# Performance work log

Measured on AMD Instinct MI355X. Metric: run time of the kernel, lower is better.

The kernel has to match this reference:

```python
import jax, jax.numpy as jnp
import numpy as np

N_NODES = 50000
N_EDGES = 800000
D = 128
N_LAYERS = 4
NUM_GRAPHS = 128
BN_EPS = 1e-5


def setup_inputs() -> dict:
    key = jax.random.key(0)
    ks = jax.random.split(key, 10)
    x = jax.random.normal(ks[0], (N_NODES, D), dtype=jnp.float32)
    edge_index = jax.random.randint(ks[1], (2, N_EDGES), 0, N_NODES, dtype=jnp.int64)
    batch = jnp.sort(jax.random.randint(ks[2], (N_NODES,), 0, NUM_GRAPHS, dtype=jnp.int64))
    # GINConv MLP params: Linear(D->D), ReLU, Linear(D->D); stacked over layers.
    scale = 1.0 / np.sqrt(D)
    W1 = jax.random.normal(ks[3], (N_LAYERS, D, D), dtype=jnp.float32) * scale
    b1 = jnp.zeros((N_LAYERS, D), dtype=jnp.float32)
    W2 = jax.random.normal(ks[4], (N_LAYERS, D, D), dtype=jnp.float32) * scale
    b2 = jnp.zeros((N_LAYERS, D), dtype=jnp.float32)
    eps = jnp.zeros((N_LAYERS,), dtype=jnp.float32)  # train_eps=True, init 0
    bn_gamma = jnp.ones((N_LAYERS - 1, D), dtype=jnp.float32)
    bn_beta = jnp.zeros((N_LAYERS - 1, D), dtype=jnp.float32)
    return {"x": x, "edge_index": edge_index, "batch": batch,
            "W1": W1, "b1": b1, "W2": W2, "b2": b2, "eps": eps,
            "bn_gamma": bn_gamma, "bn_beta": bn_beta}


def reference(x, edge_index, batch, W1, b1, W2, b2, eps, bn_gamma, bn_beta):
    src, dst = edge_index[0], edge_index[1]
    h = x
    for i in range(N_LAYERS):
        # GINConv: MLP((1+eps)*x_i + sum_{j->i} x_j)
        agg = jax.ops.segment_sum(h[src], dst, num_segments=N_NODES)  # [N, D]
        z = (1.0 + eps[i]) * h + agg
        z = jnp.maximum(z @ W1[i] + b1[i], 0.0) @ W2[i] + b2[i]
        if i < N_LAYERS - 1:
            # BatchNorm1d (training-mode batch statistics) + ReLU
            mu = jnp.mean(z, axis=0)
            var = jnp.var(z, axis=0)
            z = (z - mu) * jax.lax.rsqrt(var + BN_EPS) * bn_gamma[i] + bn_beta[i]
            z = jnp.maximum(z, 0.0)
        h = z
    # global_add_pool
    return jax.ops.segment_sum(h, batch, num_segments=NUM_GRAPHS)  # [G, D]
```

## Files before the change

### kernel.cpp

```cpp
#include <hip/hip_runtime.h>

#define N_NODES 50000
#define N_EDGES 800000
#define D 128
#define NUM_GRAPHS 128

typedef __attribute__((ext_vector_type(8)))  short bfrag8;
typedef __attribute__((ext_vector_type(16))) float f32x16;

__device__ __forceinline__ float4 f4zero() { return make_float4(0.f, 0.f, 0.f, 0.f); }

__device__ __forceinline__ unsigned short f2bf(float f) {
    unsigned u = __float_as_uint(f);
    unsigned r = (u + 0x7fffu + ((u >> 16) & 1u)) >> 16;
    return (unsigned short)r;
}
__device__ __forceinline__ float bf2f(unsigned short b) {
    return __uint_as_float(((unsigned)b) << 16);
}
__device__ __forceinline__ void acc8(float* a, uint4 r) {
    a[0] += __uint_as_float(r.x << 16);
    a[1] += __uint_as_float(r.x & 0xffff0000u);
    a[2] += __uint_as_float(r.y << 16);
    a[3] += __uint_as_float(r.y & 0xffff0000u);
    a[4] += __uint_as_float(r.z << 16);
    a[5] += __uint_as_float(r.z & 0xffff0000u);
    a[6] += __uint_as_float(r.w << 16);
    a[7] += __uint_as_float(r.w & 0xffff0000u);
}

__global__ __launch_bounds__(256) void prep_kernel(
    const float* __restrict__ W1, const float* __restrict__ W2,
    const float* __restrict__ x, short* __restrict__ Wt,
    ushort4* __restrict__ Hb, int* __restrict__ deg, float* __restrict__ stats,
    float* __restrict__ outZero)
{
    int b = blockIdx.x, t = threadIdx.x;
    if (b < 512) {
        int idx = b * 256 + t;
        int m = idx >> 14, rem = idx & 16383;
        int k = rem >> 7, n = rem & 127;
        const float* W = (m < 4) ? (W1 + (size_t)m * 16384)
                                 : (W2 + (size_t)(m - 4) * 16384);
        Wt[(size_t)m * 16384 + n * 128 + k] = (short)f2bf(W[k * 128 + n]);
    } else if (b < 6762) {
        int i = (b - 512) * 256 + t;
        float4 v = ((const float4*)x)[i];
        Hb[i] = make_ushort4(f2bf(v.x), f2bf(v.y), f2bf(v.z), f2bf(v.w));
    } else if (b < 6958) {
        int i = (b - 6762) * 256 + t;
        if (i < N_NODES) deg[i] = 0;
    } else if (b < 6982) {
        int i = (b - 6958) * 256 + t;
        stats[i] = 0.f;
    } else if (b < 7046) {
        int i = (b - 6982) * 256 + t;
        outZero[i] = 0.f;
    } else {
        if (t < 64) ((unsigned*)Hb)[(size_t)N_NODES * 64 + t] = 0u;
    }
}

__global__ __launch_bounds__(256) void hist_kernel(
    const int* __restrict__ dst, int* __restrict__ deg,
    unsigned short* __restrict__ edge_pos)
{
    int e = blockIdx.x * 256 + threadIdx.x;
    if (e < N_EDGES) edge_pos[e] = (unsigned short)atomicAdd(&deg[dst[e]], 1);
}

__global__ __launch_bounds__(256) void scan_block_kernel(
    const int* __restrict__ deg, int* __restrict__ row_ptr,
    int* __restrict__ blockSum)
{
    __shared__ int wsum[4];
    int t = threadIdx.x, b = blockIdx.x;
    int i = b * 256 + t;
    int v = (i < N_NODES) ? ((deg[i] + 7) & ~7) : 0;
    int lane = t & 63, wid = t >> 6;
    #pragma unroll
    for (int off = 1; off < 64; off <<= 1) {
        int u = __shfl_up(v, off, 64);
        if (lane >= off) v += u;
    }
    if (lane == 63) wsum[wid] = v;
    __syncthreads();
    int add = 0;
    for (int w = 0; w < wid; ++w) add += wsum[w];
    v += add;
    if (i < N_NODES) row_ptr[i + 1] = v;
    if (t == 255) blockSum[b] = v;
}

__global__ __launch_bounds__(256) void scan_fixup_kernel(
    const int* __restrict__ blockSum, int* __restrict__ row_ptr, int nb)
{
    __shared__ int wsum[4];
    __shared__ int sbuf[256];
    int t = threadIdx.x, b = blockIdx.x;
    int v = (t < nb) ? blockSum[t] : 0;
    int lane = t & 63, wid = t >> 6;
    #pragma unroll
    for (int off = 1; off < 64; off <<= 1) {
        int u = __shfl_up(v, off, 64);
        if (lane >= off) v += u;
    }
    if (lane == 63) wsum[wid] = v;
    __syncthreads();
    int add = 0;
    for (int w = 0; w < wid; ++w) add += wsum[w];
    sbuf[t] = v + add;
    __syncthreads();
    if (b == 0 && t == 0) row_ptr[0] = 0;
    if (b > 0) {
        int off = sbuf[b - 1];
        int i = b * 256 + t;
        if (i < N_NODES) row_ptr[i + 1] += off;
    }
}

__global__ __launch_bounds__(256) void fill_kernel(
    const int* __restrict__ src, const int* __restrict__ dst,
    const int* __restrict__ row_ptr, const unsigned short* __restrict__ edge_pos,
    const int* __restrict__ deg, unsigned short* __restrict__ csr_src)
{
    int b = blockIdx.x, t = threadIdx.x;
    if (b < 3125) {
        int e = b * 256 + t;
        if (e < N_EDGES)
            csr_src[row_ptr[dst[e]] + (int)edge_pos[e]] = (unsigned short)src[e];
    } else {
        int n = (b - 3125) * 256 + t;
        if (n < N_NODES) {
            int e0 = row_ptr[n] + deg[n];
            int e1 = row_ptr[n + 1];
            for (int j = e0; j < e1; ++j)
                csr_src[j] = (unsigned short)N_NODES;
        }
    }
}

__global__ __launch_bounds__(256) void bnapply_kernel(
    uint4* __restrict__ H, const float* __restrict__ stats,
    const float* __restrict__ gamma, const float* __restrict__ beta)
{
    __shared__ float sa[128], sb[128];
    int tid = threadIdx.x;
    if (tid < 128) {
        float s = 0.f, q = 0.f;
        #pragma unroll
        for (int k = 0; k < 8; ++k) {
            s += stats[k * 256 + tid];
            q += stats[k * 256 + 128 + tid];
        }
        const float invN = 1.0f / (float)N_NODES;
        float m = s * invN;
        float a = gamma[tid] * rsqrtf(q * invN - m * m + 1e-5f);
        sa[tid] = a;
        sb[tid] = beta[tid] - m * a;
    }
    __syncthreads();
    int id = blockIdx.x * 256 + tid;
    int c0 = (id & 15) * 8;
    uint4 u = H[id];
    float lo, hi;
    lo = fmaxf(sa[c0 + 0] * __uint_as_float(u.x << 16)          + sb[c0 + 0], 0.f);
    hi = fmaxf(sa[c0 + 1] * __uint_as_float(u.x & 0xffff0000u) + sb[c0 + 1], 0.f);
    u.x = (unsigned)f2bf(lo) | ((unsigned)f2bf(hi) << 16);
    lo = fmaxf(sa[c0 + 2] * __uint_as_float(u.y << 16)          + sb[c0 + 2], 0.f);
    hi = fmaxf(sa[c0 + 3] * __uint_as_float(u.y & 0xffff0000u) + sb[c0 + 3], 0.f);
    u.y = (unsigned)f2bf(lo) | ((unsigned)f2bf(hi) << 16);
    lo = fmaxf(sa[c0 + 4] * __uint_as_float(u.z << 16)          + sb[c0 + 4], 0.f);
    hi = fmaxf(sa[c0 + 5] * __uint_as_float(u.z & 0xffff0000u) + sb[c0 + 5], 0.f);
    u.z = (unsigned)f2bf(lo) | ((unsigned)f2bf(hi) << 16);
    lo = fmaxf(sa[c0 + 6] * __uint_as_float(u.w << 16)          + sb[c0 + 6], 0.f);
    hi = fmaxf(sa[c0 + 7] * __uint_as_float(u.w & 0xffff0000u) + sb[c0 + 7], 0.f);
    u.w = (unsigned)f2bf(lo) | ((unsigned)f2bf(hi) << 16);
    H[id] = u;
}

__global__ __launch_bounds__(256, 4) void gather_kernel(
    const uint4* __restrict__ H, const int* __restrict__ row_ptr,
    const unsigned short* __restrict__ csr, const float* __restrict__ epsp,
    uint4* __restrict__ A)
{
    int node = blockIdx.x * 16 + (threadIdx.x >> 4);
    int lane = threadIdx.x & 15;
    float eps1 = 1.0f + *epsp;
    int beg = row_ptr[node], end = row_ptr[node + 1];

    uint4 hv = H[(size_t)node * 16 + lane];
    float acc[8];
    acc[0] = eps1 * __uint_as_float(hv.x << 16);
    acc[1] = eps1 * __uint_as_float(hv.x & 0xffff0000u);
    acc[2] = eps1 * __uint_as_float(hv.y << 16);
    acc[3] = eps1 * __uint_as_float(hv.y & 0xffff0000u);
    acc[4] = eps1 * __uint_as_float(hv.z << 16);
    acc[5] = eps1 * __uint_as_float(hv.z & 0xffff0000u);
    acc[6] = eps1 * __uint_as_float(hv.w << 16);
    acc[7] = eps1 * __uint_as_float(hv.w & 0xffff0000u);

    int base = beg;
    int idx = (int)csr[base + lane];
    while (base < end) {
        int nb = base + 16;
        int nidx = 0;
        if (nb < end) nidx = (int)csr[nb + lane];
        int cnt = end - base;
        int s0 = __shfl(idx, 0, 16), s1 = __shfl(idx, 1, 16);
        int s2 = __shfl(idx, 2, 16), s3 = __shfl(idx, 3, 16);
        int s4 = __shfl(idx, 4, 16), s5 = __shfl(idx, 5, 16);
        int s6 = __shfl(idx, 6, 16), s7 = __shfl(idx, 7, 16);
        uint4 u0 = H[(size_t)s0 * 16 + lane];
        uint4 u1 = H[(size_t)s1 * 16 + lane];
        uint4 u2 = H[(size_t)s2 * 16 + lane];
        uint4 u3 = H[(size_t)s3 * 16 + lane];
        uint4 u4 = H[(size_t)s4 * 16 + lane];
        uint4 u5 = H[(size_t)s5 * 16 + lane];
        uint4 u6 = H[(size_t)s6 * 16 + lane];
        uint4 u7 = H[(size_t)s7 * 16 + lane];
        if (cnt > 8) {
            int t0 = __shfl(idx,  8, 16), t1 = __shfl(idx,  9, 16);
            int t2 = __shfl(idx, 10, 16), t3 = __shfl(idx, 11, 16);
            int t4 = __shfl(idx, 12, 16), t5 = __shfl(idx, 13, 16);
            int t6 = __shfl(idx, 14, 16), t7 = __shfl(idx, 15, 16);
            uint4 w0 = H[(size_t)t0 * 16 + lane];
            uint4 w1 = H[(size_t)t1 * 16 + lane];
            uint4 w2 = H[(size_t)t2 * 16 + lane];
            uint4 w3 = H[(size_t)t3 * 16 + lane];
            uint4 w4 = H[(size_t)t4 * 16 + lane];
            uint4 w5 = H[(size_t)t5 * 16 + lane];
            uint4 w6 = H[(size_t)t6 * 16 + lane];
            uint4 w7 = H[(size_t)t7 * 16 + lane];
            acc8(acc, u0); acc8(acc, u1); acc8(acc, u2); acc8(acc, u3);
            acc8(acc, u4); acc8(acc, u5); acc8(acc, u6); acc8(acc, u7);
            acc8(acc, w0); acc8(acc, w1); acc8(acc, w2); acc8(acc, w3);
            acc8(acc, w4); acc8(acc, w5); acc8(acc, w6); acc8(acc, w7);
        } else {
            acc8(acc, u0); acc8(acc, u1); acc8(acc, u2); acc8(acc, u3);
            acc8(acc, u4); acc8(acc, u5); acc8(acc, u6); acc8(acc, u7);
        }
        idx = nidx; base = nb;
    }
    uint4 o;
    o.x = (unsigned)f2bf(acc[0]) | ((unsigned)f2bf(acc[1]) << 16);
    o.y = (unsigned)f2bf(acc[2]) | ((unsigned)f2bf(acc[3]) << 16);
    o.z = (unsigned)f2bf(acc[4]) | ((unsigned)f2bf(acc[5]) << 16);
    o.w = (unsigned)f2bf(acc[6]) | ((unsigned)f2bf(acc[7]) << 16);
    A[(size_t)node * 16 + lane] = o;
}

__global__ __launch_bounds__(256, 3) void mlp_fused_kernel(
    const ushort* __restrict__ A,
    const short* __restrict__ Wt1,
    const short* __restrict__ Wt2,
    const float* __restrict__ bias1,
    const float* __restrict__ bias2,
    ushort* __restrict__ Hout,
    float* __restrict__ statsBase,
    const int* __restrict__ batch,
    float* __restrict__ poolOut,
    int M)
{
    __shared__ __align__(16) short Wlds[128 * 128];
    __shared__ __align__(16) short zlds[2][32 * 128];
    __shared__ float ssum[128];
    __shared__ float ssq[128];

    const int tid  = threadIdx.x;
    const int wv   = tid >> 6;
    const int lane = tid & 63;
    const int half = lane >> 5;
    const int ln   = lane & 31;
    const int rg   = wv & 1;
    const int ch   = wv >> 1;
    const int row0 = blockIdx.x * 64 + rg * 32;
    const bool doStats = (statsBase != nullptr);
    if (doStats && tid < 128) { ssum[tid] = 0.f; ssq[tid] = 0.f; }

    short* zw = &zlds[rg][0];

    {
        const int4* Wg = (const int4*)Wt1;
        int4* Wl = (int4*)Wlds;
        #pragma unroll
        for (int i = 0; i < 8; ++i) {
            int id = i * 256 + tid;
            int n = id >> 4, c = id & 15;
            Wl[n * 16 + (c ^ (n & 15))] = Wg[id];
        }
    }
    __syncthreads();

    {
        f32x16 acc[2];
        #pragma unroll
        for (int ci = 0; ci < 2; ++ci)
            #pragma unroll
            for (int r = 0; r < 16; ++r) acc[ci][r] = 0.f;

        bfrag8 af[8];
        int rowc = min(row0 + ln, M - 1);
        const ushort* ap = A + (size_t)rowc * 128 + half * 8;
        #pragma unroll
        for (int kk = 0; kk < 8; ++kk)
            af[kk] = *(const bfrag8*)(ap + kk * 16);

        #pragma unroll
        for (int kk = 0; kk < 8; ++kk) {
            #pragma unroll
            for (int ci = 0; ci < 2; ++ci) {
                int n = (ch * 2 + ci) * 32 + ln;
                int c = kk * 2 + half;
                bfrag8 bf = *(const bfrag8*)(Wlds + n * 128 + ((c ^ (n & 15)) << 3));
                acc[ci] = __builtin_amdgcn_mfma_f32_32x32x16_bf16(
                    af[kk], bf, acc[ci], 0, 0, 0);
            }
        }
        #pragma unroll
        for (int ci = 0; ci < 2; ++ci) {
            int col = (ch * 2 + ci) * 32 + ln;
            int cc = col >> 3, co = col & 7;
            float bv = bias1[col];
            #pragma unroll
            for (int r = 0; r < 16; ++r) {
                int rloc = (r & 3) + 8 * (r >> 2) + 4 * half;
                float v = fmaxf(acc[ci][r] + bv, 0.f);
                zw[rloc * 128 + ((cc ^ (rloc & 15)) << 3) + co] = (short)f2bf(v);
            }
        }
    }
    __syncthreads();

    bfrag8 af2[8];
    #pragma unroll
    for (int kk = 0; kk < 8; ++kk) {
        int c = kk * 2 + half;
        af2[kk] = *(const bfrag8*)(zw + ln * 128 + ((c ^ (ln & 15)) << 3));
    }
    {
        const int4* Wg = (const int4*)Wt2;
        int4* Wl = (int4*)Wlds;
        #pragma unroll
        for (int i = 0; i < 8; ++i) {
            int id = i * 256 + tid;
            int n = id >> 4, c = id & 15;
            Wl[n * 16 + (c ^ (n & 15))] = Wg[id];
        }
    }
    __syncthreads();

    {
        f32x16 acc[2];
        #pragma unroll
        for (int ci = 0; ci < 2; ++ci)
            #pragma unroll
            for (int r = 0; r < 16; ++r) acc[ci][r] = 0.f;

        #pragma unroll
        for (int kk = 0; kk < 8; ++kk) {
            #pragma unroll
            for (int ci = 0; ci < 2; ++ci) {
                int n = (ch * 2 + ci) * 32 + ln;
                int c = kk * 2 + half;
                bfrag8 bf = *(const bfrag8*)(Wlds + n * 128 + ((c ^ (n & 15)) << 3));
                acc[ci] = __builtin_amdgcn_mfma_f32_32x32x16_bf16(
                    af2[kk], bf, acc[ci], 0, 0, 0);
            }
        }
        #pragma unroll
        for (int ci = 0; ci < 2; ++ci) {
            int col = (ch * 2 + ci) * 32 + ln;
            int cc = col >> 3, co = col & 7;
            float bv = bias2[col];
            float s = 0.f, sq = 0.f;
            #pragma unroll
            for (int r = 0; r < 16; ++r) {
                int rloc = (r & 3) + 8 * (r >> 2) + 4 * half;
                float v = acc[ci][r] + bv;
                zw[rloc * 128 + ((cc ^ (rloc & 15)) << 3) + co] = (short)f2bf(v);
                if (row0 + rloc < M) { s += v; sq += v * v; }
            }
            if (doStats) {
                s  += __shfl_xor(s, 32);
                sq += __shfl_xor(sq, 32);
                if (half == 0) {
                    atomicAdd(&ssum[col], s);
                    atomicAdd(&ssq[col], sq);
                }
            }
        }
    }
    __syncthreads();

    if (poolOut == nullptr) {
        int4* Ho = (int4*)Hout;
        #pragma unroll
        for (int i = 0; i < 4; ++i) {
            int id = i * 256 + tid;
            int r = id >> 4, c = id & 15;
            int rl = r & 31;
            int grow = blockIdx.x * 64 + r;
            if (grow < M)
                Ho[(size_t)grow * 16 + c] =
                    ((const int4*)&zlds[r >> 5][0])[rl * 16 + (c ^ (rl & 15))];
        }
    } else {
        int c4 = tid & 31;
        int rl8 = tid >> 5;
        int cc = c4 >> 1, co = (c4 & 1) * 4;
        float4 ap = f4zero();
        int gcur = -1;
        for (int i = rl8; i < 64; i += 8) {
            int grow = blockIdx.x * 64 + i;
            if (grow >= M) break;
            int g = batch[grow];
            if (g != gcur) {
                if (gcur >= 0) {
                    float* o = poolOut + gcur * D + c4 * 4;
                    atomicAdd(o + 0, ap.x); atomicAdd(o + 1, ap.y);
                    atomicAdd(o + 2, ap.z); atomicAdd(o + 3, ap.w);
                }
                gcur = g; ap = f4zero();
            }
            const short* zr = &zlds[i >> 5][0];
            int rl = i & 31;
            const ushort4 u = *(const ushort4*)
                ((const ushort*)(zr + rl * 128 + ((cc ^ (rl & 15)) << 3) + co));
            ap.x += bf2f(u.x); ap.y += bf2f(u.y);
            ap.z += bf2f(u.z); ap.w += bf2f(u.w);
        }
        if (gcur >= 0) {
            float* o = poolOut + gcur * D + c4 * 4;
            atomicAdd(o + 0, ap.x); atomicAdd(o + 1, ap.y);
            atomicAdd(o + 2, ap.z); atomicAdd(o + 3, ap.w);
        }
    }
    if (doStats && tid < 128) {
        float* slot = statsBase + (size_t)(blockIdx.x & 7) * 256;
        atomicAdd(&slot[tid],       ssum[tid]);
        atomicAdd(&slot[128 + tid], ssq[tid]);
    }
}

extern "C" void kernel_launch(void* const* d_in, const int* in_sizes, int n_in,
                              void* d_out, int out_size, void* d_ws, size_t ws_size,
                              hipStream_t stream)
{
    const float* x     = (const float*)d_in[0];
    const int*   ei    = (const int*)d_in[1];
    const int*   batch = (const int*)d_in[2];
    const float* W1    = (const float*)d_in[3];
    const float* b1    = (const float*)d_in[4];
    const float* W2    = (const float*)d_in[5];
    const float* b2    = (const float*)d_in[6];
    const float* eps   = (const float*)d_in[7];
    const float* gamma = (const float*)d_in[8];
    const float* beta  = (const float*)d_in[9];
    float* out = (float*)d_out;

    unsigned short* Hb  = (unsigned short*)d_ws;
    unsigned short* Abf = Hb + (size_t)(N_NODES + 1) * D;
    float* stats    = (float*)(Abf + (size_t)N_NODES * D);
    int*   deg      = (int*)(stats + 3 * 2048);
    int*   row_ptr  = deg + N_NODES;
    int*   blockSum = row_ptr + N_NODES + 1;
    unsigned short* edge_pos = (unsigned short*)(blockSum + 256);
    unsigned short* csr_src  = edge_pos + N_EDGES;
    short* Wt       = (short*)(csr_src + N_EDGES + 7 * N_NODES + 16);

    const int* src = ei;
    const int* dst = ei + N_EDGES;

    const int edgeBlocks   = (N_EDGES + 255) / 256;
    const int scanBlocks   = (N_NODES + 255) / 256;
    const int gatherBlocks = (N_NODES + 15) / 16;
    const int bnBlocks     = (N_NODES * 16) / 256;
    const int gemmBlocks   = (N_NODES + 63) / 64;

    prep_kernel<<<7047, 256, 0, stream>>>(W1, W2, x, Wt, (ushort4*)Hb,
                                          deg, stats, out);
    hist_kernel<<<edgeBlocks, 256, 0, stream>>>(dst, deg, edge_pos);
    scan_block_kernel<<<scanBlocks, 256, 0, stream>>>(deg, row_ptr, blockSum);
    scan_fixup_kernel<<<scanBlocks, 256, 0, stream>>>(blockSum, row_ptr, scanBlocks);
    fill_kernel<<<edgeBlocks + scanBlocks, 256, 0, stream>>>(
        src, dst, row_ptr, edge_pos, deg, csr_src);

    for (int layer = 0; layer < 4; ++layer) {
        const bool bn = (layer < 3);
        if (layer > 0) {
            bnapply_kernel<<<bnBlocks, 256, 0, stream>>>(
                (uint4*)Hb, stats + (size_t)(layer - 1) * 2048,
                gamma + (size_t)(layer - 1) * D, beta + (size_t)(layer - 1) * D);
        }
        gather_kernel<<<gatherBlocks, 256, 0, stream>>>(
            (const uint4*)Hb, row_ptr, csr_src, eps + layer, (uint4*)Abf);
        mlp_fused_kernel<<<gemmBlocks, 256, 0, stream>>>(
            Abf, Wt + (size_t)layer * 16384, Wt + (size_t)(4 + layer) * 16384,
            b1 + (size_t)layer * D, b2 + (size_t)layer * D, Hb,
            bn ? stats + (size_t)layer * 2048 : nullptr,
            bn ? nullptr : batch,
            bn ? nullptr : out, N_NODES);
    }
}
```

Baseline: 360.9 us.

## Fuse neighbor gather into the MLP kernel with ping-pong feature buffers

The separate gather kernel is removed. Each MLP block now aggregates neighbor features for its own 64 rows straight into swizzled LDS, and the MFMA A-fragments are read from LDS instead of from a global intermediate. Input and output node buffers alternate between layers so the fused kernel never overwrites features other blocks are still gathering from. This saves one launch per layer and the write and re-read of the aggregated matrix. In exchange, the latency-bound gather now runs at the GEMM kernel's lower occupancy (launch bounds of 3 waves' worth of blocks instead of 4) and is not overlapped with the MFMA work.

```diff
diff --git a/kernel.cpp b/kernel.cpp
--- a/kernel.cpp
+++ b/kernel.cpp
@@ -32,7 +32,8 @@
 __global__ __launch_bounds__(256) void prep_kernel(
     const float* __restrict__ W1, const float* __restrict__ W2,
     const float* __restrict__ x, short* __restrict__ Wt,
-    ushort4* __restrict__ Hb, int* __restrict__ deg, float* __restrict__ stats,
+    ushort4* __restrict__ Hb, unsigned* __restrict__ HcDummy,
+    int* __restrict__ deg, float* __restrict__ stats,
     float* __restrict__ outZero)
 {
     int b = blockIdx.x, t = threadIdx.x;
@@ -57,7 +58,8 @@
         int i = (b - 6982) * 256 + t;
         outZero[i] = 0.f;
     } else {
-        if (t < 64) ((unsigned*)Hb)[(size_t)N_NODES * 64 + t] = 0u;
+        if (t < 64)       ((unsigned*)Hb)[(size_t)N_NODES * 64 + t] = 0u;
+        else if (t < 128) HcDummy[t - 64] = 0u;
     }
 }
 
@@ -179,79 +181,11 @@
     H[id] = u;
 }
 
-__global__ __launch_bounds__(256, 4) void gather_kernel(
-    const uint4* __restrict__ H, const int* __restrict__ row_ptr,
-    const unsigned short* __restrict__ csr, const float* __restrict__ epsp,
-    uint4* __restrict__ A)
-{
-    int node = blockIdx.x * 16 + (threadIdx.x >> 4);
-    int lane = threadIdx.x & 15;
-    float eps1 = 1.0f + *epsp;
-    int beg = row_ptr[node], end = row_ptr[node + 1];
-
-    uint4 hv = H[(size_t)node * 16 + lane];
-    float acc[8];
-    acc[0] = eps1 * __uint_as_float(hv.x << 16);
-    acc[1] = eps1 * __uint_as_float(hv.x & 0xffff0000u);
-    acc[2] = eps1 * __uint_as_float(hv.y << 16);
-    acc[3] = eps1 * __uint_as_float(hv.y & 0xffff0000u);
-    acc[4] = eps1 * __uint_as_float(hv.z << 16);
-    acc[5] = eps1 * __uint_as_float(hv.z & 0xffff0000u);
-    acc[6] = eps1 * __uint_as_float(hv.w << 16);
-    acc[7] = eps1 * __uint_as_float(hv.w & 0xffff0000u);
-
-    int base = beg;
-    int idx = (int)csr[base + lane];
-    while (base < end) {
-        int nb = base + 16;
-        int nidx = 0;
-        if (nb < end) nidx = (int)csr[nb + lane];
-        int cnt = end - base;
-        int s0 = __shfl(idx, 0, 16), s1 = __shfl(idx, 1, 16);
-        int s2 = __shfl(idx, 2, 16), s3 = __shfl(idx, 3, 16);
-        int s4 = __shfl(idx, 4, 16), s5 = __shfl(idx, 5, 16);
-        int s6 = __shfl(idx, 6, 16), s7 = __shfl(idx, 7, 16);
-        uint4 u0 = H[(size_t)s0 * 16 + lane];
-        uint4 u1 = H[(size_t)s1 * 16 + lane];
-        uint4 u2 = H[(size_t)s2 * 16 + lane];
-        uint4 u3 = H[(size_t)s3 * 16 + lane];
-        uint4 u4 = H[(size_t)s4 * 16 + lane];
-        uint4 u5 = H[(size_t)s5 * 16 + lane];
-        uint4 u6 = H[(size_t)s6 * 16 + lane];
-        uint4 u7 = H[(size_t)s7 * 16 + lane];
-        if (cnt > 8) {
-            int t0 = __shfl(idx,  8, 16), t1 = __shfl(idx,  9, 16);
-            int t2 = __shfl(idx, 10, 16), t3 = __shfl(idx, 11, 16);
-            int t4 = __shfl(idx, 12, 16), t5 = __shfl(idx, 13, 16);
-            int t6 = __shfl(idx, 14, 16), t7 = __shfl(idx, 15, 16);
-            uint4 w0 = H[(size_t)t0 * 16 + lane];
-            uint4 w1 = H[(size_t)t1 * 16 + lane];
-            uint4 w2 = H[(size_t)t2 * 16 + lane];
-            uint4 w3 = H[(size_t)t3 * 16 + lane];
-            uint4 w4 = H[(size_t)t4 * 16 + lane];
-            uint4 w5 = H[(size_t)t5 * 16 + lane];
-            uint4 w6 = H[(size_t)t6 * 16 + lane];
-            uint4 w7 = H[(size_t)t7 * 16 + lane];
-            acc8(acc, u0); acc8(acc, u1); acc8(acc, u2); acc8(acc, u3);
-            acc8(acc, u4); acc8(acc, u5); acc8(acc, u6); acc8(acc, u7);
-            acc8(acc, w0); acc8(acc, w1); acc8(acc, w2); acc8(acc, w3);
-            acc8(acc, w4); acc8(acc, w5); acc8(acc, w6); acc8(acc, w7);
-        } else {
-            acc8(acc, u0); acc8(acc, u1); acc8(acc, u2); acc8(acc, u3);
-            acc8(acc, u4); acc8(acc, u5); acc8(acc, u6); acc8(acc, u7);
-        }
-        idx = nidx; base = nb;
-    }
-    uint4 o;
-    o.x = (unsigned)f2bf(acc[0]) | ((unsigned)f2bf(acc[1]) << 16);
-    o.y = (unsigned)f2bf(acc[2]) | ((unsigned)f2bf(acc[3]) << 16);
-    o.z = (unsigned)f2bf(acc[4]) | ((unsigned)f2bf(acc[5]) << 16);
-    o.w = (unsigned)f2bf(acc[6]) | ((unsigned)f2bf(acc[7]) << 16);
-    A[(size_t)node * 16 + lane] = o;
-}
-
-__global__ __launch_bounds__(256, 3) void mlp_fused_kernel(
-    const ushort* __restrict__ A,
+__global__ __launch_bounds__(256, 3) void layer_kernel(
+    const ushort* __restrict__ Hin,
+    const int* __restrict__ row_ptr,
+    const unsigned short* __restrict__ csr,
+    const float* __restrict__ epsp,
     const short* __restrict__ Wt1,
     const short* __restrict__ Wt2,
     const float* __restrict__ bias1,
@@ -281,6 +215,86 @@
     short* zw = &zlds[rg][0];
 
     {
+        const uint4* H4 = (const uint4*)Hin;
+        const float eps1 = 1.0f + *epsp;
+        const int gl = tid & 15;
+        #pragma unroll
+        for (int it = 0; it < 4; ++it) {
+            int r = it * 16 + (tid >> 4);
+            int node = blockIdx.x * 64 + r;
+            float acc[8] = {0.f, 0.f, 0.f, 0.f, 0.f, 0.f, 0.f, 0.f};
+            if (node < M) {
+                uint4 hv = H4[(size_t)node * 16 + gl];
+                acc[0] = eps1 * __uint_as_float(hv.x << 16);
+                acc[1] = eps1 * __uint_as_float(hv.x & 0xffff0000u);
+                acc[2] = eps1 * __uint_as_float(hv.y << 16);
+                acc[3] = eps1 * __uint_as_float(hv.y & 0xffff0000u);
+                acc[4] = eps1 * __uint_as_float(hv.z << 16);
+                acc[5] = eps1 * __uint_as_float(hv.z & 0xffff0000u);
+                acc[6] = eps1 * __uint_as_float(hv.w << 16);
+                acc[7] = eps1 * __uint_as_float(hv.w & 0xffff0000u);
+                int beg = row_ptr[node], end = row_ptr[node + 1];
+                int base = beg;
+                int idx = (int)csr[base + gl];
+                while (base < end) {
+                    int nb = base + 16;
+                    int nidx = 0;
+                    if (nb < end) nidx = (int)csr[nb + gl];
+                    int cnt = end - base;
+                    int s0 = __shfl(idx, 0, 16), s1 = __shfl(idx, 1, 16);
+                    int s2 = __shfl(idx, 2, 16), s3 = __shfl(idx, 3, 16);
+                    int s4 = __shfl(idx, 4, 16), s5 = __shfl(idx, 5, 16);
+                    int s6 = __shfl(idx, 6, 16), s7 = __shfl(idx, 7, 16);
+                    uint4 u0 = H4[(size_t)s0 * 16 + gl];
+                    uint4 u1 = H4[(size_t)s1 * 16 + gl];
+                    uint4 u2 = H4[(size_t)s2 * 16 + gl];
+                    uint4 u3 = H4[(size_t)s3 * 16 + gl];
+                    uint4 u4 = H4[(size_t)s4 * 16 + gl];
+                    uint4 u5 = H4[(size_t)s5 * 16 + gl];
+                    uint4 u6 = H4[(size_t)s6 * 16 + gl];
+                    uint4 u7 = H4[(size_t)s7 * 16 + gl];
+                    if (cnt > 8) {
+                        int t0 = __shfl(idx,  8, 16), t1 = __shfl(idx,  9, 16);
+                        int t2 = __shfl(idx, 10, 16), t3 = __shfl(idx, 11, 16);
+                        int t4 = __shfl(idx, 12, 16), t5 = __shfl(idx, 13, 16);
+                        int t6 = __shfl(idx, 14, 16), t7 = __shfl(idx, 15, 16);
+                        uint4 w0 = H4[(size_t)t0 * 16 + gl];
+                        uint4 w1 = H4[(size_t)t1 * 16 + gl];
+                        uint4 w2 = H4[(size_t)t2 * 16 + gl];
+                        uint4 w3 = H4[(size_t)t3 * 16 + gl];
+                        uint4 w4 = H4[(size_t)t4 * 16 + gl];
+                        uint4 w5 = H4[(size_t)t5 * 16 + gl];
+                        uint4 w6 = H4[(size_t)t6 * 16 + gl];
+                        uint4 w7 = H4[(size_t)t7 * 16 + gl];
+                        acc8(acc, u0); acc8(acc, u1); acc8(acc, u2); acc8(acc, u3);
+                        acc8(acc, u4); acc8(acc, u5); acc8(acc, u6); acc8(acc, u7);
+                        acc8(acc, w0); acc8(acc, w1); acc8(acc, w2); acc8(acc, w3);
+                        acc8(acc, w4); acc8(acc, w5); acc8(acc, w6); acc8(acc, w7);
+                    } else {
+                        acc8(acc, u0); acc8(acc, u1); acc8(acc, u2); acc8(acc, u3);
+                        acc8(acc, u4); acc8(acc, u5); acc8(acc, u6); acc8(acc, u7);
+                    }
+                    idx = nidx; base = nb;
+                }
+            }
+            uint4 o;
+            o.x = (unsigned)f2bf(acc[0]) | ((unsigned)f2bf(acc[1]) << 16);
+            o.y = (unsigned)f2bf(acc[2]) | ((unsigned)f2bf(acc[3]) << 16);
+            o.z = (unsigned)f2bf(acc[4]) | ((unsigned)f2bf(acc[5]) << 16);
+            o.w = (unsigned)f2bf(acc[6]) | ((unsigned)f2bf(acc[7]) << 16);
+            int rl = r & 31;
+            ((uint4*)&zlds[r >> 5][0])[rl * 16 + (gl ^ (rl & 15))] = o;
+        }
+    }
+    __syncthreads();
+
+    bfrag8 af[8];
+    #pragma unroll
+    for (int kk = 0; kk < 8; ++kk) {
+        int c = kk * 2 + half;
+        af[kk] = *(const bfrag8*)(zw + ln * 128 + ((c ^ (ln & 15)) << 3));
+    }
+    {
         const int4* Wg = (const int4*)Wt1;
         int4* Wl = (int4*)Wlds;
         #pragma unroll
@@ -298,13 +312,6 @@
         for (int ci = 0; ci < 2; ++ci)
             #pragma unroll
             for (int r = 0; r < 16; ++r) acc[ci][r] = 0.f;
-
-        bfrag8 af[8];
-        int rowc = min(row0 + ln, M - 1);
-        const ushort* ap = A + (size_t)rowc * 128 + half * 8;
-        #pragma unroll
-        for (int kk = 0; kk < 8; ++kk)
-            af[kk] = *(const bfrag8*)(ap + kk * 16);
 
         #pragma unroll
         for (int kk = 0; kk < 8; ++kk) {
@@ -460,8 +467,8 @@
     float* out = (float*)d_out;
 
     unsigned short* Hb  = (unsigned short*)d_ws;
-    unsigned short* Abf = Hb + (size_t)(N_NODES + 1) * D;
-    float* stats    = (float*)(Abf + (size_t)N_NODES * D);
+    unsigned short* Hc  = Hb + (size_t)(N_NODES + 1) * D;
+    float* stats    = (float*)(Hc + (size_t)(N_NODES + 1) * D);
     int*   deg      = (int*)(stats + 3 * 2048);
     int*   row_ptr  = deg + N_NODES;
     int*   blockSum = row_ptr + N_NODES + 1;
@@ -472,13 +479,13 @@
     const int* src = ei;
     const int* dst = ei + N_EDGES;
 
-    const int edgeBlocks   = (N_EDGES + 255) / 256;
-    const int scanBlocks   = (N_NODES + 255) / 256;
-    const int gatherBlocks = (N_NODES + 15) / 16;
-    const int bnBlocks     = (N_NODES * 16) / 256;
-    const int gemmBlocks   = (N_NODES + 63) / 64;
+    const int edgeBlocks = (N_EDGES + 255) / 256;
+    const int scanBlocks = (N_NODES + 255) / 256;
+    const int bnBlocks   = (N_NODES * 16) / 256;
+    const int gemmBlocks = (N_NODES + 63) / 64;
 
     prep_kernel<<<7047, 256, 0, stream>>>(W1, W2, x, Wt, (ushort4*)Hb,
+                                          (unsigned*)(Hc + (size_t)N_NODES * D),
                                           deg, stats, out);
     hist_kernel<<<edgeBlocks, 256, 0, stream>>>(dst, deg, edge_pos);
     scan_block_kernel<<<scanBlocks, 256, 0, stream>>>(deg, row_ptr, blockSum);
@@ -486,20 +493,22 @@
     fill_kernel<<<edgeBlocks + scanBlocks, 256, 0, stream>>>(
         src, dst, row_ptr, edge_pos, deg, csr_src);
 
+    unsigned short* Hin  = Hb;
+    unsigned short* HoutB = Hc;
     for (int layer = 0; layer < 4; ++layer) {
         const bool bn = (layer < 3);
         if (layer > 0) {
             bnapply_kernel<<<bnBlocks, 256, 0, stream>>>(
-                (uint4*)Hb, stats + (size_t)(layer - 1) * 2048,
+                (uint4*)Hin, stats + (size_t)(layer - 1) * 2048,
                 gamma + (size_t)(layer - 1) * D, beta + (size_t)(layer - 1) * D);
         }
-        gather_kernel<<<gatherBlocks, 256, 0, stream>>>(
-            (const uint4*)Hb, row_ptr, csr_src, eps + layer, (uint4*)Abf);
-        mlp_fused_kernel<<<gemmBlocks, 256, 0, stream>>>(
-            Abf, Wt + (size_t)layer * 16384, Wt + (size_t)(4 + layer) * 16384,
-            b1 + (size_t)layer * D, b2 + (size_t)layer * D, Hb,
+        layer_kernel<<<gemmBlocks, 256, 0, stream>>>(
+            Hin, row_ptr, csr_src, eps + layer,
+            Wt + (size_t)layer * 16384, Wt + (size_t)(4 + layer) * 16384,
+            b1 + (size_t)layer * D, b2 + (size_t)layer * D, HoutB,
             bn ? stats + (size_t)layer * 2048 : nullptr,
             bn ? nullptr : batch,
             bn ? nullptr : out, N_NODES);
-    }
-}
+        unsigned short* tmp = Hin; Hin = HoutB; HoutB = tmp;
+    }
+}
```

Result: faster. 342.7 us, median of 2 (-5.0%).
